# Performance work log

Measured on AMD Instinct MI355X. Metric: run time of the kernel, lower is better.

## Reference

```python
import jax, jax.numpy as jnp
import numpy as np

BETA = 0.25
ENTROPY_LOSS_RATIO = 0.1
TEMPERATURE = 0.01
EPS = 1e-5


def _l2norm(x):
    return x / jnp.sqrt(jnp.sum(x * x, axis=-1, keepdims=True)).clip(1e-12)


def _entropy_loss(affinity):
    # affinity: [N, n_e]
    a = affinity / TEMPERATURE
    probs = jax.nn.softmax(a, axis=-1)
    log_probs = jax.nn.log_softmax(a + EPS, axis=-1)
    avg_probs = jnp.mean(probs, axis=0)
    avg_entropy = -jnp.sum(avg_probs * jnp.log(avg_probs + EPS))
    sample_entropy = -jnp.mean(jnp.sum(probs * log_probs, axis=-1))
    return sample_entropy - avg_entropy


def setup_inputs() -> dict:
    key = jax.random.key(0)
    k1, k2, k3 = jax.random.split(key, 3)
    B, C, H, W = 16, 256, 32, 32
    n_e = 16384
    z = jax.random.normal(k1, (B, C, H, W), dtype=jnp.float32)
    embedding = jax.random.normal(k2, (n_e, C), dtype=jnp.float32) * 0.02
    query_ids = jax.random.randint(k3, (B, 1), 0, W, dtype=jnp.int64)
    return {"z": z, "embedding": embedding, "query_ids": query_ids}


def reference(z, embedding, query_ids):
    B, C, H, W = z.shape
    sg = jax.lax.stop_gradient
    zt = jnp.transpose(z, (0, 2, 3, 1))            # [B,H,W,C]
    # l2_norm=True path
    zt = _l2norm(zt)
    emb = _l2norm(embedding)                       # [n_e, C]
    zf = zt.reshape(-1, C)                         # [N, C]
    d = (jnp.sum(zf * zf, axis=1, keepdims=True)
         + jnp.sum(emb * emb, axis=1)
         - 2.0 * jnp.einsum('nd,kd->nk', zf, emb))  # [N, n_e]
    idx = jnp.argmin(d, axis=1)                    # [N]
    z_q = emb[idx].reshape(zt.shape)               # [B,H,W,C]

    # dead code rate (unbiased std over batch, per token position)
    code = idx.reshape(B, -1).astype(jnp.float32)
    dead_code_rate = jnp.mean((jnp.std(code, axis=0, ddof=1) < 1e-5).astype(jnp.float32))

    vq_loss = jnp.mean((z_q - sg(zt)) ** 2, axis=-1, keepdims=True)      # [B,H,W,1]
    commit_loss = BETA * jnp.mean((sg(z_q) - zt) ** 2, axis=-1, keepdims=True)
    loss_mask = (jnp.arange(W).reshape(1, 1, -1, 1)
                 <= query_ids[:, -1].reshape(-1, 1, 1, 1)).astype(jnp.float32)
    denom = jnp.sum(loss_mask)
    vq_loss = jnp.sum(vq_loss * loss_mask) / denom
    commit_loss = jnp.sum(commit_loss * loss_mask) / denom
    entropy_loss = ENTROPY_LOSS_RATIO * _entropy_loss(-d)

    # straight-through estimator
    z_q_st = zt + sg(z_q - zt)
    z_q_out = jnp.transpose(z_q_st, (0, 3, 1, 2))  # [B,C,H,W]
    return (z_q_out, vq_loss, commit_loss, entropy_loss, dead_code_rate, idx)
```

## Files before the change

kernel.cpp:

```cpp
#include <hip/hip_runtime.h>
#include <math.h>

#define N_TOK   16384
#define N_E     16384
#define CDIM    256
#define NCH     8
#define CHSZ    (N_E / NCH)
#define L2E100  144.26950408889634f
#define DELTA_C 0.06f
#define DELTA_D 0.03f
#define EPS_NT  0.008f
#define CAP_BLK 1536u
#define NT_CAP  65536u

typedef __attribute__((ext_vector_type(8))) short short8;
typedef __attribute__((ext_vector_type(4))) float f32x4;

#define OFF_A2   0u
#define OFF_B2   2097152u
#define OFF_RMX  4194304u
#define OFF_CS   4210688u
#define OFF_SC   4227072u
#define OFF_RK   4227088u
#define OFF_NT   4259856u
#define OFF_NTC  4325392u
#define OFF_CBC  4325408u
#define OFF_IDX  4327456u
#define OFF_CAND 4343840u
#define OFF_ZT   10635296u
#define NEED_ZT_BYTES 59318400ull

__device__ __forceinline__ unsigned short f2bf(float x) {
  unsigned u = __float_as_uint(x);
  unsigned r = (u + 0x7fffu + ((u >> 16) & 1u)) >> 16;
  return (unsigned short)r;
}
__device__ __forceinline__ float bf2f(unsigned short h) {
  return __uint_as_float(((unsigned)h) << 16);
}
__device__ __forceinline__ unsigned fkey(float f) {
  unsigned u = __float_as_uint(f);
  return (u & 0x80000000u) ? ~u : (u | 0x80000000u);
}
__device__ __forceinline__ float keyf(unsigned k) {
  return (k & 0x80000000u) ? __uint_as_float(k ^ 0x80000000u) : __uint_as_float(~k);
}

__device__ __forceinline__ void async_load16(const void* g, void* l) {
  __builtin_amdgcn_global_load_lds((const __attribute__((address_space(1))) void*)g,
                                   (__attribute__((address_space(3))) void*)l, 16, 0, 0);
}

__device__ __forceinline__ float blockReduceSum256(float v, float* sbuf) {
  __syncthreads();
  v += __shfl_down(v, 32);
  v += __shfl_down(v, 16);
  v += __shfl_down(v, 8);
  v += __shfl_down(v, 4);
  v += __shfl_down(v, 2);
  v += __shfl_down(v, 1);
  const int tid = threadIdx.x;
  if ((tid & 63) == 0) sbuf[tid >> 6] = v;
  __syncthreads();
  return sbuf[0] + sbuf[1] + sbuf[2] + sbuf[3];
}

__global__ __launch_bounds__(256) void k_norm_emb(const float* __restrict__ emb,
    unsigned short* __restrict__ B2, float* __restrict__ colsum,
    float* __restrict__ scalars, unsigned long long* __restrict__ rowkey,
    unsigned* __restrict__ ntc, unsigned* __restrict__ rowMaxU) {
  const int tid = threadIdx.x, lane = tid & 63, wv = tid >> 6;
  if (blockIdx.x < 64) {
    const int i = blockIdx.x * 256 + tid;
    colsum[i] = 0.f;
    rowkey[i] = ~0ull;
    rowMaxU[i] = 0u;
    if (i < 16) { scalars[i] = 0.f; ntc[i] = 0u; }
  }
  const int k = blockIdx.x * 4 + wv;
  const float4 v = *(const float4*)&emb[(size_t)k * CDIM + lane * 4];
  float ss = v.x * v.x + v.y * v.y + v.z * v.z + v.w * v.w;
#pragma unroll
  for (int off = 1; off < 64; off <<= 1) ss += __shfl_xor(ss, off);
  const float r = 1.0f / fmaxf(sqrtf(ss), 1e-12f);
  ushort4 o;
  o.x = f2bf(v.x * r); o.y = f2bf(v.y * r);
  o.z = f2bf(v.z * r); o.w = f2bf(v.w * r);
  *(ushort4*)&B2[(size_t)k * CDIM + lane * 4] = o;
}

__global__ __launch_bounds__(256) void k_norm_z(const float* __restrict__ z,
                                                unsigned short* __restrict__ A2,
                                                float* __restrict__ zT) {
  __shared__ float ssb[4][64];
  __shared__ float rn[64];
  __shared__ unsigned short tile[64 * 264];
  __shared__ float tileF[64 * 260];
  const int b = blockIdx.x >> 4, hw0 = (blockIdx.x & 15) * 64;
  const int tid = threadIdx.x, cg = tid >> 6, hwl = tid & 63;
  float ss = 0.f;
#pragma unroll 8
  for (int i = 0; i < 64; ++i) {
    const int c = cg + i * 4;
    const float x = z[((size_t)(b * CDIM + c) << 10) + hw0 + hwl];
    ss = fmaf(x, x, ss);
  }
  ssb[cg][hwl] = ss;
  __syncthreads();
  if (tid < 64) {
    const float t = ssb[0][tid] + ssb[1][tid] + ssb[2][tid] + ssb[3][tid];
    rn[tid] = 1.0f / fmaxf(sqrtf(t), 1e-12f);
  }
  __syncthreads();
  const float r = rn[hwl];
#pragma unroll 8
  for (int i = 0; i < 64; ++i) {
    const int c = cg + i * 4;
    const float x = z[((size_t)(b * CDIM + c) << 10) + hw0 + hwl];
    tile[hwl * 264 + c] = f2bf(x * r);
    tileF[hwl * 260 + c] = x;
  }
  __syncthreads();
  const int rr = tid >> 5, tt = tid & 31;
#pragma unroll
  for (int it = 0; it < 8; ++it) {
    const int row = rr + 8 * it;
    const int token = b * 1024 + hw0 + row;
    const uint4 v = *(const uint4*)&tile[row * 264 + tt * 8];
    *(uint4*)&A2[(size_t)token * CDIM + tt * 8] = v;
    if (zT != nullptr) {
      const float4 f0 = *(const float4*)&tileF[row * 260 + tt * 4];
      const float4 f1 = *(const float4*)&tileF[row * 260 + 128 + tt * 4];
      *(float4*)&zT[(size_t)token * CDIM + tt * 4] = f0;
      *(float4*)&zT[(size_t)token * CDIM + 128 + tt * 4] = f1;
    }
  }
}

__global__ __launch_bounds__(256, 4) void k_pass1(const unsigned short* __restrict__ A2,
    const unsigned short* __restrict__ B2,
    unsigned long long* __restrict__ cand, unsigned* __restrict__ cbc,
    unsigned* __restrict__ rowMaxU) {
  __shared__ alignas(16) unsigned short Bt[2][128 * 32];
  __shared__ unsigned lcnt;
  const int rt = blockIdx.x, chunk = blockIdx.y;
  const int r0 = rt * 64, k0 = chunk * CHSZ;
  const int blin = rt * NCH + chunk;
  const int tid = threadIdx.x, lane = tid & 63, w = tid >> 6;
  const int wr0 = w * 16;
  const int l15 = lane & 15, quad = lane >> 4;

  if (tid == 0) lcnt = 0u;

  short8 afr[8];
  {
    const size_t rbase = (size_t)(r0 + wr0 + l15) * CDIM;
#pragma unroll
    for (int j = 0; j < 8; ++j)
      afr[j] = *(const short8*)&A2[rbase + j * 32 + quad * 8];
  }

  const unsigned short* bsrc[2];
  unsigned bdst[2];
#pragma unroll
  for (int i = 0; i < 2; ++i) {
    const int lin = i * 256 + tid;
    const int row = lin >> 2, slot = lin & 3;
    const int gcg = slot ^ ((row >> 1) & 3);
    bsrc[i] = B2 + (size_t)(k0 + row) * CDIM + gcg * 8;
    bdst[i] = (unsigned)lin * 16u;
  }

  int boff[8];
#pragma unroll
  for (int tj = 0; tj < 8; ++tj) {
    const int br = tj * 16 + l15;
    boff[tj] = br * 32 + ((quad ^ ((br >> 1) & 3)) * 8);
  }

#pragma unroll
  for (int i = 0; i < 2; ++i)
    async_load16(bsrc[i], (char*)Bt[0] + bdst[i]);
  __syncthreads();

  f32x4 acc[8];
  float runMax[4];
#pragma unroll
  for (int r = 0; r < 4; ++r) runMax[r] = -3.0e38f;

#pragma unroll 1
  for (int ct = 0; ct < 16; ++ct) {
#pragma unroll
    for (int tj = 0; tj < 8; ++tj) acc[tj] = (f32x4){0.f, 0.f, 0.f, 0.f};

#pragma unroll
    for (int st = 0; st < 8; ++st) {
      if (!(ct == 15 && st == 7)) {
        const int noff = (st < 7) ? (ct * 32768 + (st + 1) * 32)
                                  : ((ct + 1) * 32768);
        char* dbuf = (char*)Bt[(st + 1) & 1];
#pragma unroll
        for (int i = 0; i < 2; ++i)
          async_load16(bsrc[i] + noff, dbuf + bdst[i]);
      }
      const unsigned short* bp = Bt[st & 1];
      short8 bfr[8];
#pragma unroll
      for (int tj = 0; tj < 8; ++tj)
        bfr[tj] = *(const short8*)&bp[boff[tj]];
#pragma unroll
      for (int tj = 0; tj < 8; ++tj)
        acc[tj] = __builtin_amdgcn_mfma_f32_16x16x32_bf16(afr[st], bfr[tj],
                                                          acc[tj], 0, 0, 0);

      if (st == 7) {
        const int kb = k0 + ct * 128;
#pragma unroll
        for (int r = 0; r < 4; ++r) {
          float mt = acc[0][r];
#pragma unroll
          for (int tj = 1; tj < 8; ++tj) mt = fmaxf(mt, acc[tj][r]);
          mt = fmaxf(mt, __shfl_xor(mt, 1));
          mt = fmaxf(mt, __shfl_xor(mt, 2));
          mt = fmaxf(mt, __shfl_xor(mt, 4));
          mt = fmaxf(mt, __shfl_xor(mt, 8));
          runMax[r] = fmaxf(runMax[r], mt);
          const float thrD = runMax[r] - DELTA_D;
          const unsigned rowg = (unsigned)(r0 + wr0 + quad * 4 + r);
#pragma unroll
          for (int tj = 0; tj < 8; ++tj) {
            const float d = acc[tj][r];
            if (d >= thrD) {
              const unsigned slot = atomicAdd(&lcnt, 1u);
              if (slot < CAP_BLK) {
                const float t = d + d;
                const unsigned pr = (rowg << 14) | (unsigned)(kb + tj * 16 + l15);
                cand[(size_t)blin * CAP_BLK + slot] =
                    ((unsigned long long)__float_as_uint(t) << 32) | pr;
              }
            }
          }
        }
      }
      __syncthreads();
    }
  }

#pragma unroll
  for (int r = 0; r < 4; ++r)
    if (l15 == 0)
      atomicMax(&rowMaxU[r0 + wr0 + quad * 4 + r], fkey(runMax[r] + runMax[r]));
  if (tid == 0) cbc[blin] = lcnt < CAP_BLK ? lcnt : CAP_BLK;
}

__global__ __launch_bounds__(256) void k_cstat2(const unsigned long long* __restrict__ cand,
    const unsigned* __restrict__ cbc, const unsigned* __restrict__ rowMaxU,
    float* __restrict__ colsum, unsigned* __restrict__ ntList,
    unsigned* __restrict__ ntc, float* __restrict__ scalars) {
  __shared__ float lM[64], lZ[64], lE[64], lIZ[64];
  __shared__ float sbuf[4];
  const int rt = blockIdx.x, r0 = rt * 64;
  const int tid = threadIdx.x, lane = tid & 63;
  if (tid < 64) {
    lM[tid] = keyf(rowMaxU[r0 + tid]);
    lZ[tid] = 0.f; lE[tid] = 0.f;
  }
  __syncthreads();
  for (int sub = 0; sub < NCH; ++sub) {
    const int blin = rt * NCH + sub;
    const unsigned cnt = cbc[blin] < CAP_BLK ? cbc[blin] : CAP_BLK;
    for (unsigned i = tid; i < cnt; i += 256u) {
      const unsigned long long e = cand[(size_t)blin * CAP_BLK + i];
      const unsigned pr = (unsigned)(e & 0xFFFFFFFu);
      const float t = __uint_as_float((unsigned)(e >> 32));
      const int rowl = (int)((pr >> 14) & 63u);
      const float d = t - lM[rowl];
      const float ex = exp2f(d * L2E100);
      atomicAdd(&lZ[rowl], ex);
      atomicAdd(&lE[rowl], d * 100.0f * ex);
    }
  }
  __syncthreads();
  float ent = 0.f;
  if (tid < 64) {
    const float Z = lZ[tid];
    lIZ[tid] = 1.0f / Z;
    ent = logf(Z) - lE[tid] / Z;
  }
  const float es = blockReduceSum256(ent, sbuf);
  if (tid == 0) atomicAdd(&scalars[1], es);
  __syncthreads();
  for (int sub = 0; sub < NCH; ++sub) {
    const int blin = rt * NCH + sub;
    const unsigned cnt = cbc[blin] < CAP_BLK ? cbc[blin] : CAP_BLK;
    const unsigned lim = (cnt + 255u) & ~255u;
    for (unsigned i = tid; i < lim; i += 256u) {
      bool nt = false;
      unsigned pr = 0u;
      if (i < cnt) {
        const unsigned long long e = cand[(size_t)blin * CAP_BLK + i];
        pr = (unsigned)(e & 0xFFFFFFFu);
        const float t = __uint_as_float((unsigned)(e >> 32));
        const int rowl = (int)((pr >> 14) & 63u);
        const float d = t - lM[rowl];
        atomicAdd(&colsum[pr & 0x3FFFu], exp2f(d * L2E100) * lIZ[rowl]);
        nt = (d >= -EPS_NT);
      }
      const unsigned long long mask = __ballot(nt);
      const unsigned cw = (unsigned)__popcll(mask);
      unsigned base = 0u;
      if (lane == 0 && cw) base = atomicAdd(ntc, cw);
      base = __shfl((int)base, 0);
      if (nt) {
        const unsigned off = (unsigned)__popcll(mask & ((1ull << lane) - 1ull));
        const unsigned s = base + off;
        if (s < NT_CAP) ntList[s] = pr;
      }
    }
  }
}

__global__ __launch_bounds__(256) void k_refine(const float* __restrict__ z,
    const float* __restrict__ zT, const float* __restrict__ emb,
    const unsigned* __restrict__ ntList, const unsigned* __restrict__ ntc,
    unsigned long long* __restrict__ rowkey) {
  const unsigned cnt = *ntc;
  const unsigned lim = cnt < NT_CAP ? cnt : NT_CAP;
  const int lane = threadIdx.x & 63, wv = threadIdx.x >> 6;
  for (unsigned slot = blockIdx.x * 4 + wv; slot < lim; slot += gridDim.x * 4) {
    const unsigned pr = ntList[slot];
    const int n = (int)(pr >> 14), k = (int)(pr & 0x3FFFu);
    const int b = n >> 10, hw = n & 1023;
    double sz = 0.0, se = 0.0, sp = 0.0;
#pragma unroll
    for (int u = 0; u < CDIM / 64; ++u) {
      const int c = lane + u * 64;
      const double zv = (zT != nullptr)
          ? (double)zT[(size_t)n * CDIM + c]
          : (double)z[((size_t)(b * CDIM + c) << 10) + hw];
      const double ev = (double)emb[(size_t)k * CDIM + c];
      sz = fma(zv, zv, sz); se = fma(ev, ev, se); sp = fma(zv, ev, sp);
    }
    for (int off = 32; off; off >>= 1) {
      sz += __shfl_down(sz, off);
      se += __shfl_down(se, off);
      sp += __shfl_down(sp, off);
    }
    if (lane == 0) {
      const double nz = fmax(sqrt(sz), 1e-12);
      const double ne = fmax(sqrt(se), 1e-12);
      const double d = sz / (nz * nz) + se / (ne * ne) - 2.0 * sp / (nz * ne);
      const unsigned long long key =
          (((unsigned long long)(d * 140737488355328.0)) << 14) | (unsigned long long)k;
      atomicMin(&rowkey[n], key);
    }
  }
}

__global__ __launch_bounds__(256) void k_zq(const unsigned short* __restrict__ A2,
    const unsigned short* __restrict__ B2, const unsigned long long* __restrict__ rowkey,
    const long long* __restrict__ qids, int* __restrict__ idxI,
    float* __restrict__ outIdxF, float* __restrict__ outZ,
    float* __restrict__ scalars) {
  __shared__ int lidx[64];
  __shared__ unsigned short tile[64 * 264];
  __shared__ float sbuf[4];
  const int b = blockIdx.x >> 4, hw0 = (blockIdx.x & 15) * 64;
  const int tid = threadIdx.x;
  if (tid < 64) {
    const int n = b * 1024 + hw0 + tid;
    const unsigned long long key = rowkey[n];
    const int k = (key != ~0ull) ? (int)(key & 0x3FFFull) : 0;
    lidx[tid] = k;
    idxI[n] = k;
    outIdxF[n] = (float)k;
  }
  __syncthreads();
  const long long qid = qids[b];
  const int rr = tid >> 5, tt = tid & 31;
  float vq = 0.f;
#pragma unroll
  for (int it = 0; it < 8; ++it) {
    const int row = rr + 8 * it;
    const int token = b * 1024 + hw0 + row;
    union { uint4 v; unsigned short s[8]; } ev, zv;
    ev.v = *(const uint4*)&B2[(size_t)lidx[row] * CDIM + tt * 8];
    zv.v = *(const uint4*)&A2[(size_t)token * CDIM + tt * 8];
    *(uint4*)&tile[row * 264 + tt * 8] = ev.v;
    float dd = 0.f;
#pragma unroll
    for (int u = 0; u < 8; ++u) {
      const float d = bf2f(ev.s[u]) - bf2f(zv.s[u]);
      dd = fmaf(d, d, dd);
    }
    if ((long long)(row & 31) <= qid) vq += dd;
  }
  const float s = blockReduceSum256(vq, sbuf);
  if (tid == 0) atomicAdd(&scalars[0], s * (1.0f / 256.0f));
  __syncthreads();
  const int cg = tid >> 6, hwl = tid & 63;
#pragma unroll 8
  for (int i = 0; i < 64; ++i) {
    const int c = cg + i * 4;
    outZ[((size_t)(b * CDIM + c) << 10) + hw0 + hwl] = bf2f(tile[hwl * 264 + c]);
  }
}

__global__ __launch_bounds__(256) void k_final(const int* __restrict__ idxI,
    const long long* __restrict__ qids, const float* __restrict__ colsum,
    const float* __restrict__ scalars, float* __restrict__ out) {
  __shared__ float sbuf[4];
  const int tid = threadIdx.x;
  float ae = 0.f;
  for (int i = tid; i < N_E; i += 256) {
    const float q = colsum[i] * (1.0f / (float)N_TOK);
    ae += q * logf(q + 1e-5f);
  }
  const float aes = blockReduceSum256(ae, sbuf);
  int cnt = 0;
  for (int p = tid; p < 1024; p += 256) {
    const int v = idxI[p];
    bool eq = true;
    for (int b = 1; b < 16; ++b) eq = eq && (idxI[b * 1024 + p] == v);
    cnt += eq ? 1 : 0;
  }
  const float dc = blockReduceSum256((float)cnt, sbuf);
  if (tid == 0) {
    float denom = 0.f;
    for (int b = 0; b < 16; ++b) denom += (float)(qids[b] + 1ll);
    out[4194304] = scalars[0] / denom;
    out[4194305] = 0.25f * scalars[0] / denom;
    out[4194306] = 0.1f * (scalars[1] * (1.0f / (float)N_TOK) + aes);
    out[4194307] = dc * (1.0f / 1024.0f);
  }
}

extern "C" void kernel_launch(void* const* d_in, const int* in_sizes, int n_in,
                              void* d_out, int out_size, void* d_ws, size_t ws_size,
                              hipStream_t stream) {
  const float*      z    = (const float*)d_in[0];
  const float*      emb  = (const float*)d_in[1];
  const long long*  qids = (const long long*)d_in[2];
  float* out = (float*)d_out;
  float* W   = (float*)d_ws;

  unsigned short* A2 = (unsigned short*)(W + OFF_A2);
  unsigned short* B2 = (unsigned short*)(W + OFF_B2);
  unsigned* rowMaxU = (unsigned*)(W + OFF_RMX);
  float* colsum = W + OFF_CS;
  float* scal   = W + OFF_SC;
  unsigned long long* rowkey = (unsigned long long*)(W + OFF_RK);
  unsigned* ntList = (unsigned*)(W + OFF_NT);
  unsigned* ntc    = (unsigned*)(W + OFF_NTC);
  unsigned* cbc    = (unsigned*)(W + OFF_CBC);
  int* idxI        = (int*)(W + OFF_IDX);
  unsigned long long* cand = (unsigned long long*)(W + OFF_CAND);
  float* zT = (ws_size >= NEED_ZT_BYTES) ? (W + OFF_ZT) : (float*)nullptr;

  k_norm_emb<<<dim3(N_E / 4),     dim3(256), 0, stream>>>(emb, B2, colsum, scal,
                                                          rowkey, ntc, rowMaxU);
  k_norm_z  <<<dim3(256),         dim3(256), 0, stream>>>(z, A2, zT);
  k_pass1   <<<dim3(256, NCH),    dim3(256), 0, stream>>>(A2, B2, cand, cbc, rowMaxU);
  k_cstat2  <<<dim3(256),         dim3(256), 0, stream>>>(cand, cbc, rowMaxU, colsum,
                                                          ntList, ntc, scal);
  k_refine  <<<dim3(1024),        dim3(256), 0, stream>>>(z, zT, emb, ntList, ntc, rowkey);
  k_zq      <<<dim3(256),         dim3(256), 0, stream>>>(A2, B2, rowkey, qids,
                                                          idxI, out + 4194308, out, scal);
  k_final   <<<dim3(1),           dim3(256), 0, stream>>>(idxI, qids, colsum, scal, out);
}
```

Before: 549.8 us.

## Double row tile per block in pass1 to reuse each B tile across 128 rows

Each k_pass1 block now covers 128 token rows instead of 64, with each wave holding two 16-row A fragments and running 16 MFMAs per staged B tile. This halves the grid and halves the global-to-LDS traffic for the codebook per row, raising arithmetic intensity. Candidate counters are split into two per-half-block slots so the downstream candidate layout stays the same. The cost is twice the accumulator and A-fragment registers, so launch bounds drop from 4 to 3 blocks per CU, which lowers occupancy and leaves fewer blocks (1024) to spread across the CUs.

Result: slower. 702.0 us (+27.7%).

```diff
diff --git a/kernel.cpp b/kernel.cpp
--- a/kernel.cpp
+++ b/kernel.cpp
@@ -7,7 +7,6 @@
 #define NCH     8
 #define CHSZ    (N_E / NCH)
 #define L2E100  144.26950408889634f
-#define DELTA_C 0.06f
 #define DELTA_D 0.03f
 #define EPS_NT  0.008f
 #define CAP_BLK 1536u
@@ -137,27 +136,32 @@
   }
 }
 
-__global__ __launch_bounds__(256, 4) void k_pass1(const unsigned short* __restrict__ A2,
+__global__ __launch_bounds__(256, 3) void k_pass1(const unsigned short* __restrict__ A2,
     const unsigned short* __restrict__ B2,
     unsigned long long* __restrict__ cand, unsigned* __restrict__ cbc,
     unsigned* __restrict__ rowMaxU) {
   __shared__ alignas(16) unsigned short Bt[2][128 * 32];
-  __shared__ unsigned lcnt;
+  __shared__ unsigned lcntA, lcntB;
   const int rt = blockIdx.x, chunk = blockIdx.y;
-  const int r0 = rt * 64, k0 = chunk * CHSZ;
-  const int blin = rt * NCH + chunk;
+  const int r0 = rt * 128, k0 = chunk * CHSZ;
+  const int blinA = (2 * rt) * NCH + chunk;
+  const int blinB = (2 * rt + 1) * NCH + chunk;
   const int tid = threadIdx.x, lane = tid & 63, w = tid >> 6;
-  const int wr0 = w * 16;
+  const int wr0 = w * 32;
   const int l15 = lane & 15, quad = lane >> 4;
 
-  if (tid == 0) lcnt = 0u;
-
-  short8 afr[8];
-  {
-    const size_t rbase = (size_t)(r0 + wr0 + l15) * CDIM;
+  if (tid == 0) lcntA = 0u;
+  if (tid == 128) lcntB = 0u;
+  const int myBlin = (w < 2) ? blinA : blinB;
+  unsigned* myCnt = (w < 2) ? &lcntA : &lcntB;
+
+  short8 afr[2][8];
+#pragma unroll
+  for (int ti = 0; ti < 2; ++ti) {
+    const size_t rbase = (size_t)(r0 + wr0 + ti * 16 + l15) * CDIM;
 #pragma unroll
     for (int j = 0; j < 8; ++j)
-      afr[j] = *(const short8*)&A2[rbase + j * 32 + quad * 8];
+      afr[ti][j] = *(const short8*)&A2[rbase + j * 32 + quad * 8];
   }
 
   const unsigned short* bsrc[2];
@@ -183,15 +187,19 @@
     async_load16(bsrc[i], (char*)Bt[0] + bdst[i]);
   __syncthreads();
 
-  f32x4 acc[8];
-  float runMax[4];
-#pragma unroll
-  for (int r = 0; r < 4; ++r) runMax[r] = -3.0e38f;
+  f32x4 acc[2][8];
+  float runMax[2][4];
+#pragma unroll
+  for (int ti = 0; ti < 2; ++ti)
+#pragma unroll
+    for (int r = 0; r < 4; ++r) runMax[ti][r] = -3.0e38f;
 
 #pragma unroll 1
   for (int ct = 0; ct < 16; ++ct) {
 #pragma unroll
-    for (int tj = 0; tj < 8; ++tj) acc[tj] = (f32x4){0.f, 0.f, 0.f, 0.f};
+    for (int ti = 0; ti < 2; ++ti)
+#pragma unroll
+      for (int tj = 0; tj < 8; ++tj) acc[ti][tj] = (f32x4){0.f, 0.f, 0.f, 0.f};
 
 #pragma unroll
     for (int st = 0; st < 8; ++st) {
@@ -209,48 +217,57 @@
       for (int tj = 0; tj < 8; ++tj)
         bfr[tj] = *(const short8*)&bp[boff[tj]];
 #pragma unroll
-      for (int tj = 0; tj < 8; ++tj)
-        acc[tj] = __builtin_amdgcn_mfma_f32_16x16x32_bf16(afr[st], bfr[tj],
-                                                          acc[tj], 0, 0, 0);
+      for (int ti = 0; ti < 2; ++ti)
+#pragma unroll
+        for (int tj = 0; tj < 8; ++tj)
+          acc[ti][tj] = __builtin_amdgcn_mfma_f32_16x16x32_bf16(afr[ti][st], bfr[tj],
+                                                                acc[ti][tj], 0, 0, 0);
 
       if (st == 7) {
         const int kb = k0 + ct * 128;
 #pragma unroll
-        for (int r = 0; r < 4; ++r) {
-          float mt = acc[0][r];
-#pragma unroll
-          for (int tj = 1; tj < 8; ++tj) mt = fmaxf(mt, acc[tj][r]);
-          mt = fmaxf(mt, __shfl_xor(mt, 1));
-          mt = fmaxf(mt, __shfl_xor(mt, 2));
-          mt = fmaxf(mt, __shfl_xor(mt, 4));
-          mt = fmaxf(mt, __shfl_xor(mt, 8));
-          runMax[r] = fmaxf(runMax[r], mt);
-          const float thrD = runMax[r] - DELTA_D;
-          const unsigned rowg = (unsigned)(r0 + wr0 + quad * 4 + r);
-#pragma unroll
-          for (int tj = 0; tj < 8; ++tj) {
-            const float d = acc[tj][r];
-            if (d >= thrD) {
-              const unsigned slot = atomicAdd(&lcnt, 1u);
-              if (slot < CAP_BLK) {
-                const float t = d + d;
-                const unsigned pr = (rowg << 14) | (unsigned)(kb + tj * 16 + l15);
-                cand[(size_t)blin * CAP_BLK + slot] =
-                    ((unsigned long long)__float_as_uint(t) << 32) | pr;
+        for (int ti = 0; ti < 2; ++ti)
+#pragma unroll
+          for (int r = 0; r < 4; ++r) {
+            float mt = acc[ti][0][r];
+#pragma unroll
+            for (int tj = 1; tj < 8; ++tj) mt = fmaxf(mt, acc[ti][tj][r]);
+            mt = fmaxf(mt, __shfl_xor(mt, 1));
+            mt = fmaxf(mt, __shfl_xor(mt, 2));
+            mt = fmaxf(mt, __shfl_xor(mt, 4));
+            mt = fmaxf(mt, __shfl_xor(mt, 8));
+            runMax[ti][r] = fmaxf(runMax[ti][r], mt);
+            const float thrD = runMax[ti][r] - DELTA_D;
+            const unsigned rowg = (unsigned)(r0 + wr0 + ti * 16 + quad * 4 + r);
+#pragma unroll
+            for (int tj = 0; tj < 8; ++tj) {
+              const float d = acc[ti][tj][r];
+              if (d >= thrD) {
+                const unsigned slot = atomicAdd(myCnt, 1u);
+                if (slot < CAP_BLK) {
+                  const float t = d + d;
+                  const unsigned pr = (rowg << 14) | (unsigned)(kb + tj * 16 + l15);
+                  cand[(size_t)myBlin * CAP_BLK + slot] =
+                      ((unsigned long long)__float_as_uint(t) << 32) | pr;
+                }
               }
             }
           }
-        }
       }
       __syncthreads();
     }
   }
 
 #pragma unroll
-  for (int r = 0; r < 4; ++r)
-    if (l15 == 0)
-      atomicMax(&rowMaxU[r0 + wr0 + quad * 4 + r], fkey(runMax[r] + runMax[r]));
-  if (tid == 0) cbc[blin] = lcnt < CAP_BLK ? lcnt : CAP_BLK;
+  for (int ti = 0; ti < 2; ++ti)
+#pragma unroll
+    for (int r = 0; r < 4; ++r)
+      if (l15 == 0)
+        atomicMax(&rowMaxU[r0 + wr0 + ti * 16 + quad * 4 + r],
+                  fkey(runMax[ti][r] + runMax[ti][r]));
+  __syncthreads();
+  if (tid == 0)   cbc[blinA] = lcntA < CAP_BLK ? lcntA : CAP_BLK;
+  if (tid == 128) cbc[blinB] = lcntB < CAP_BLK ? lcntB : CAP_BLK;
 }
 
 __global__ __launch_bounds__(256) void k_cstat2(const unsigned long long* __restrict__ cand,
@@ -460,7 +477,7 @@
   k_norm_emb<<<dim3(N_E / 4),     dim3(256), 0, stream>>>(emb, B2, colsum, scal,
                                                           rowkey, ntc, rowMaxU);
   k_norm_z  <<<dim3(256),         dim3(256), 0, stream>>>(z, A2, zT);
-  k_pass1   <<<dim3(256, NCH),    dim3(256), 0, stream>>>(A2, B2, cand, cbc, rowMaxU);
+  k_pass1   <<<dim3(128, NCH),    dim3(256), 0, stream>>>(A2, B2, cand, cbc, rowMaxU);
   k_cstat2  <<<dim3(256),         dim3(256), 0, stream>>>(cand, cbc, rowMaxU, colsum,
                                                           ntList, ntc, scal);
   k_refine  <<<dim3(1024),        dim3(256), 0, stream>>>(z, zT, emb, ntList, ntc, rowkey);
```
